# Performance work log

Hardware: AMD Instinct MI355X
Metric: run time of the kernel (lower is better)

## Reference

```python
import jax, jax.numpy as jnp
import numpy as np


def _backwarp(img, flow):
    """Bilinear backward warp of img [B,C,H,W] by flow [B,2,H,W] (pixels).
    Matches torch grid_sample(mode='bilinear', padding_mode='zeros', align_corners=False)
    with the standard softmax-splatting backwarp grid construction."""
    B, C, H, W = img.shape
    # normalized base grid (align_corners=False convention used by backwarp)
    hor = jnp.linspace(-1.0 + 1.0 / W, 1.0 - 1.0 / W, W, dtype=img.dtype)  # [W]
    ver = jnp.linspace(-1.0 + 1.0 / H, 1.0 - 1.0 / H, H, dtype=img.dtype)  # [H]
    gx = hor[None, None, :] + flow[:, 0] / ((W - 1.0) / 2.0)  # [B,H,W]
    gy = ver[None, :, None] + flow[:, 1] / ((H - 1.0) / 2.0)  # [B,H,W]
    # unnormalize (align_corners=False): x = ((g+1)*size - 1)/2
    ix = ((gx + 1.0) * W - 1.0) * 0.5
    iy = ((gy + 1.0) * H - 1.0) * 0.5
    x0 = jnp.floor(ix)
    y0 = jnp.floor(iy)
    wx1 = ix - x0
    wy1 = iy - y0
    wx0 = 1.0 - wx1
    wy0 = 1.0 - wy1

    flat = img.reshape(B, C, H * W)

    def gather(xi, yi):
        valid = (xi >= 0) & (xi <= W - 1) & (yi >= 0) & (yi <= H - 1)  # [B,H,W]
        xc = jnp.clip(xi, 0, W - 1).astype(jnp.int32)
        yc = jnp.clip(yi, 0, H - 1).astype(jnp.int32)
        idx = (yc * W + xc).reshape(B, 1, H * W)
        v = jnp.take_along_axis(flat, jnp.broadcast_to(idx, (B, C, H * W)), axis=2)
        return v.reshape(B, C, H, W) * valid[:, None].astype(img.dtype)

    x1 = x0 + 1.0
    y1 = y0 + 1.0
    out = (gather(x0, y0) * (wy0 * wx0)[:, None]
           + gather(x1, y0) * (wy0 * wx1)[:, None]
           + gather(x0, y1) * (wy1 * wx0)[:, None]
           + gather(x1, y1) * (wy1 * wx1)[:, None])
    return out


def setup_inputs() -> dict:
    key = jax.random.key(0)
    k1, k2, k3 = jax.random.split(key, 3)
    B, C, H, W = 16, 3, 768, 1024
    ten_first = jax.random.normal(k1, (B, C, H, W), dtype=jnp.float32)
    ten_second = jax.random.normal(k2, (B, C, H, W), dtype=jnp.float32)
    tenFlow = jax.random.normal(k3, (B, 2, H, W), dtype=jnp.float32)
    alpha = -jnp.ones((1, 1, 1, 1), dtype=jnp.float32)  # learnable scale, init -1
    return {"ten_first": ten_first, "ten_second": ten_second, "tenFlow": tenFlow, "alpha": alpha}


def reference(ten_first, ten_second, tenFlow, alpha):
    warped = _backwarp(ten_second, tenFlow)
    l1 = jnp.abs(ten_first - warped)                       # [B,C,H,W]
    return alpha * jnp.mean(l1, axis=1, keepdims=True)     # [B,1,H,W]
```

## Files before the change

kernel.cpp:

```cpp
#include <hip/hip_runtime.h>

constexpr int B  = 16;
constexpr int C  = 3;
constexpr int H  = 768;
constexpr int W  = 1024;
constexpr int HW = H * W;

__global__ __launch_bounds__(256) void warp_l1_mean_kernel(
    const float* __restrict__ first,
    const float* __restrict__ second,
    const float* __restrict__ flow,
    const float* __restrict__ alpha,
    float* __restrict__ out)
{
    const int gid = blockIdx.x * blockDim.x + threadIdx.x;
    if (gid >= B * HW) return;

    const int b = gid / HW;
    const int p = gid - b * HW;
    const int y = p / W;
    const int x = p - y * W;

    const float* fl = flow + (size_t)b * 2 * HW;
    const float fx = fl[p];
    const float fy = fl[HW + p];

    const float ix = (float)x + fx * ((float)W / (float)(W - 1));
    const float iy = (float)y + fy * ((float)H / (float)(H - 1));

    const float x0f = floorf(ix);
    const float y0f = floorf(iy);
    const float wx1 = ix - x0f;
    const float wy1 = iy - y0f;
    const float wx0 = 1.0f - wx1;
    const float wy0 = 1.0f - wy1;

    const int x0 = (int)x0f;
    const int y0 = (int)y0f;
    const int x1 = x0 + 1;
    const int y1 = y0 + 1;

    const bool vx0 = (x0 >= 0) && (x0 <= W - 1);
    const bool vx1 = (x1 >= 0) && (x1 <= W - 1);
    const bool vy0 = (y0 >= 0) && (y0 <= H - 1);
    const bool vy1 = (y1 >= 0) && (y1 <= H - 1);

    const int cx0 = min(max(x0, 0), W - 1);
    const int cx1 = min(max(x1, 0), W - 1);
    const int cy0 = min(max(y0, 0), H - 1);
    const int cy1 = min(max(y1, 0), H - 1);

    const float w00 = wy0 * wx0 * ((vx0 && vy0) ? 1.0f : 0.0f);
    const float w01 = wy0 * wx1 * ((vx1 && vy0) ? 1.0f : 0.0f);
    const float w10 = wy1 * wx0 * ((vx0 && vy1) ? 1.0f : 0.0f);
    const float w11 = wy1 * wx1 * ((vx1 && vy1) ? 1.0f : 0.0f);

    const int i00 = cy0 * W + cx0;
    const int i01 = cy0 * W + cx1;
    const int i10 = cy1 * W + cx0;
    const int i11 = cy1 * W + cx1;

    const float* sec = second + (size_t)b * C * HW;
    const float* fst = first  + (size_t)b * C * HW;
    const float a = alpha[0];

    float acc = 0.0f;
#pragma unroll
    for (int c = 0; c < C; ++c) {
        const float* s = sec + c * HW;
        const float warped = w00 * s[i00] + w01 * s[i01]
                           + w10 * s[i10] + w11 * s[i11];
        acc += fabsf(fst[c * HW + p] - warped);
    }

    out[gid] = a * (acc * (1.0f / 3.0f));
}

extern "C" void kernel_launch(void* const* d_in, const int* in_sizes, int n_in,
                              void* d_out, int out_size, void* d_ws, size_t ws_size,
                              hipStream_t stream) {
    const float* first  = (const float*)d_in[0];
    const float* second = (const float*)d_in[1];
    const float* flow   = (const float*)d_in[2];
    const float* alpha  = (const float*)d_in[3];
    float* out = (float*)d_out;

    const int total = B * HW;
    const int block = 256;
    const int grid  = (total + block - 1) / block;

    warp_l1_mean_kernel<<<grid, block, 0, stream>>>(first, second, flow, alpha, out);
}
```

Before: 409.2 us.

## Stage warp source tiles with halo in LDS and remap blocks across XCDs

Each block now handles a 64x16 output tile and first loads the corresponding region of the second image, plus a 5-pixel halo, into shared memory for all three channels. Bilinear taps whose footprint falls inside the tile read from LDS; the rest fall back to global gathers. Block indices are remapped so neighbouring tiles land on the same XCD, which should improve L2 locality. The cost is redundant halo loading, a barrier per block, and a slow path for large flows.

```diff
diff --git a/kernel.cpp b/kernel.cpp
--- a/kernel.cpp
+++ b/kernel.cpp
@@ -6,74 +6,131 @@
 constexpr int W  = 1024;
 constexpr int HW = H * W;
 
-__global__ __launch_bounds__(256) void warp_l1_mean_kernel(
+constexpr int TX = 64;
+constexpr int TY = 16;
+constexpr int R  = 5;
+constexpr int TCOLS = TX + 2 * R + 1;
+constexpr int TROWS = TY + 2 * R + 1;
+constexpr int TSTR  = TCOLS + 1;
+constexpr int NXT = W / TX;
+constexpr int NYT = H / TY;
+constexpr int NWG = B * NXT * NYT;
+constexpr int NXCD = 8;
+constexpr int PERX = NWG / NXCD;
+
+__global__ __launch_bounds__(256) void warp_l1_mean_tiled(
     const float* __restrict__ first,
     const float* __restrict__ second,
     const float* __restrict__ flow,
     const float* __restrict__ alpha,
     float* __restrict__ out)
 {
-    const int gid = blockIdx.x * blockDim.x + threadIdx.x;
-    if (gid >= B * HW) return;
+    __shared__ float tile[C][TROWS][TSTR];
 
-    const int b = gid / HW;
-    const int p = gid - b * HW;
-    const int y = p / W;
-    const int x = p - y * W;
+    const int hw  = blockIdx.x;
+    const int wid = (hw & (NXCD - 1)) * PERX + (hw >> 3);
 
-    const float* fl = flow + (size_t)b * 2 * HW;
-    const float fx = fl[p];
-    const float fy = fl[HW + p];
+    const int b   = wid / (NXT * NYT);
+    const int r0  = wid - b * (NXT * NYT);
+    const int tyi = r0 / NXT;
+    const int txi = r0 - tyi * NXT;
 
-    const float ix = (float)x + fx * ((float)W / (float)(W - 1));
-    const float iy = (float)y + fy * ((float)H / (float)(H - 1));
+    const int x_base = txi * TX;
+    const int y_base = tyi * TY;
+    const int x_lo   = x_base - R;
+    const int y_lo   = y_base - R;
 
-    const float x0f = floorf(ix);
-    const float y0f = floorf(iy);
-    const float wx1 = ix - x0f;
-    const float wy1 = iy - y0f;
-    const float wx0 = 1.0f - wx1;
-    const float wy0 = 1.0f - wy1;
+    const float* __restrict__ sec = second + (size_t)b * C * HW;
+    const float* __restrict__ fst = first  + (size_t)b * C * HW;
+    const float* __restrict__ fl  = flow   + (size_t)b * 2 * HW;
+    float*       __restrict__ op  = out    + (size_t)b * HW;
 
-    const int x0 = (int)x0f;
-    const int y0 = (int)y0f;
-    const int x1 = x0 + 1;
-    const int y1 = y0 + 1;
+    for (int j = threadIdx.x; j < TROWS * TCOLS; j += 256) {
+        const int r  = j / TCOLS;
+        const int cc = j - r * TCOLS;
+        const int gx = min(max(x_lo + cc, 0), W - 1);
+        const int gy = min(max(y_lo + r,  0), H - 1);
+        const int idx = gy * W + gx;
+        tile[0][r][cc] = sec[idx];
+        tile[1][r][cc] = sec[HW + idx];
+        tile[2][r][cc] = sec[2 * HW + idx];
+    }
+    __syncthreads();
 
-    const bool vx0 = (x0 >= 0) && (x0 <= W - 1);
-    const bool vx1 = (x1 >= 0) && (x1 <= W - 1);
-    const bool vy0 = (y0 >= 0) && (y0 <= H - 1);
-    const bool vy1 = (y1 >= 0) && (y1 <= H - 1);
-
-    const int cx0 = min(max(x0, 0), W - 1);
-    const int cx1 = min(max(x1, 0), W - 1);
-    const int cy0 = min(max(y0, 0), H - 1);
-    const int cy1 = min(max(y1, 0), H - 1);
-
-    const float w00 = wy0 * wx0 * ((vx0 && vy0) ? 1.0f : 0.0f);
-    const float w01 = wy0 * wx1 * ((vx1 && vy0) ? 1.0f : 0.0f);
-    const float w10 = wy1 * wx0 * ((vx0 && vy1) ? 1.0f : 0.0f);
-    const float w11 = wy1 * wx1 * ((vx1 && vy1) ? 1.0f : 0.0f);
-
-    const int i00 = cy0 * W + cx0;
-    const int i01 = cy0 * W + cx1;
-    const int i10 = cy1 * W + cx0;
-    const int i11 = cy1 * W + cx1;
-
-    const float* sec = second + (size_t)b * C * HW;
-    const float* fst = first  + (size_t)b * C * HW;
+    const int px  = threadIdx.x & 63;
+    const int py0 = threadIdx.x >> 6;
+    const int x   = x_base + px;
     const float a = alpha[0];
 
-    float acc = 0.0f;
 #pragma unroll
-    for (int c = 0; c < C; ++c) {
-        const float* s = sec + c * HW;
-        const float warped = w00 * s[i00] + w01 * s[i01]
-                           + w10 * s[i10] + w11 * s[i11];
-        acc += fabsf(fst[c * HW + p] - warped);
+    for (int k = 0; k < 4; ++k) {
+        const int y = y_base + py0 + 4 * k;
+        const int p = y * W + x;
+
+        const float fx = fl[p];
+        const float fy = fl[HW + p];
+
+        const float ix = (float)x + fx * ((float)W / (float)(W - 1));
+        const float iy = (float)y + fy * ((float)H / (float)(H - 1));
+
+        const float x0f = floorf(ix);
+        const float y0f = floorf(iy);
+        const float wx1 = ix - x0f;
+        const float wy1 = iy - y0f;
+        const float wx0 = 1.0f - wx1;
+        const float wy0 = 1.0f - wy1;
+
+        const int x0 = (int)x0f;
+        const int y0 = (int)y0f;
+        const int x1 = x0 + 1;
+        const int y1 = y0 + 1;
+
+        const bool vx0 = (x0 >= 0) && (x0 < W);
+        const bool vx1 = (x1 >= 0) && (x1 < W);
+        const bool vy0 = (y0 >= 0) && (y0 < H);
+        const bool vy1 = (y1 >= 0) && (y1 < H);
+
+        const float w00 = wy0 * wx0 * ((vx0 && vy0) ? 1.0f : 0.0f);
+        const float w01 = wy0 * wx1 * ((vx1 && vy0) ? 1.0f : 0.0f);
+        const float w10 = wy1 * wx0 * ((vx0 && vy1) ? 1.0f : 0.0f);
+        const float w11 = wy1 * wx1 * ((vx1 && vy1) ? 1.0f : 0.0f);
+
+        const int lx = x0 - x_lo;
+        const int ly = y0 - y_lo;
+
+        float acc = 0.0f;
+        if ((unsigned)lx < (unsigned)(TCOLS - 1) &&
+            (unsigned)ly < (unsigned)(TROWS - 1)) {
+#pragma unroll
+            for (int c = 0; c < C; ++c) {
+                const float* tp = &tile[c][ly][lx];
+                const float v00 = tp[0];
+                const float v01 = tp[1];
+                const float v10 = tp[TSTR];
+                const float v11 = tp[TSTR + 1];
+                const float warped = w00 * v00 + w01 * v01 + w10 * v10 + w11 * v11;
+                acc += fabsf(fst[c * HW + p] - warped);
+            }
+        } else {
+            const int cx0 = min(max(x0, 0), W - 1);
+            const int cx1 = min(max(x1, 0), W - 1);
+            const int cy0 = min(max(y0, 0), H - 1);
+            const int cy1 = min(max(y1, 0), H - 1);
+            const int i00 = cy0 * W + cx0;
+            const int i01 = cy0 * W + cx1;
+            const int i10 = cy1 * W + cx0;
+            const int i11 = cy1 * W + cx1;
+#pragma unroll
+            for (int c = 0; c < C; ++c) {
+                const float* s = sec + c * HW;
+                const float warped = w00 * s[i00] + w01 * s[i01]
+                                   + w10 * s[i10] + w11 * s[i11];
+                acc += fabsf(fst[c * HW + p] - warped);
+            }
+        }
+
+        op[p] = a * (acc * (1.0f / 3.0f));
     }
-
-    out[gid] = a * (acc * (1.0f / 3.0f));
 }
 
 extern "C" void kernel_launch(void* const* d_in, const int* in_sizes, int n_in,
@@ -85,9 +142,5 @@
     const float* alpha  = (const float*)d_in[3];
     float* out = (float*)d_out;
 
-    const int total = B * HW;
-    const int block = 256;
-    const int grid  = (total + block - 1) / block;
-
-    warp_l1_mean_kernel<<<grid, block, 0, stream>>>(first, second, flow, alpha, out);
+    warp_l1_mean_tiled<<<NWG, 256, 0, stream>>>(first, second, flow, alpha, out);
 }
```

Result: faster. 392.3 us (-4.1%).
